# Performance work log

Measured on AMD Instinct MI355X. Metric: run time of the kernel, lower is better.

Reference implementation:

```python
import jax, jax.numpy as jnp
import numpy as np
import math

LN_EPS = 1e-5
EPS = 1e-8

def _unfold3(x, stride):
    # torch nn.Unfold(kernel_size=3, stride=stride, padding=1); output [B, C*9, L]
    B, C, H, W = x.shape
    xp = jnp.pad(x, ((0, 0), (0, 0), (1, 1), (1, 1)))
    Ho = (H + 2 - 3) // stride + 1
    Wo = (W + 2 - 3) // stride + 1
    pats = [xp[:, :, i:i + stride * (Ho - 1) + 1:stride, j:j + stride * (Wo - 1) + 1:stride]
            for i in range(3) for j in range(3)]
    out = jnp.stack(pats, axis=2)  # [B,C,9,Ho,Wo]  (c-major, then kh,kw: torch ordering)
    return out.reshape(B, C * 9, Ho * Wo)

def _ln(x, g, b):
    mu = jnp.mean(x, axis=-1, keepdims=True)
    var = jnp.mean((x - mu) ** 2, axis=-1, keepdims=True)
    return (x - mu) * jax.lax.rsqrt(var + LN_EPS) * g + b

def _prm_exp(x, w):
    # x: [B,T,emb], w: [m,emb] -> [B,T,m]
    m = w.shape[0]
    xd = jnp.sum(x * x, axis=-1, keepdims=True) / 2.0
    wtx = jnp.einsum('bte,me->btm', x, w)
    return jnp.exp(wtx - xd) / math.sqrt(m)

def _performer(x, kqv_w, kqv_b, pw, pb, g1, b1, g2, b2, m1w, m1b, m2w, m2b, w):
    # Token_performer.forward (dropout = identity, eval mode)
    h = _ln(x, g1, b1)
    kqv = h @ kqv_w.T + kqv_b
    k, q, v = jnp.split(kqv, 3, axis=-1)  # torch.split order: k, q, v
    kp = _prm_exp(k, w)
    qp = _prm_exp(q, w)
    D = jnp.einsum('btm,bm->bt', qp, kp.sum(axis=1))[..., None]        # [B,T,1]
    kptv = jnp.einsum('btn,btm->bnm', v, kp)                            # [B,emb,m]
    y = jnp.einsum('btm,bnm->btn', qp, kptv) / (D + EPS)                # [B,T,emb]
    y = v + (y @ pw.T + pb)
    h2 = _ln(y, g2, b2)
    mlp = jax.nn.gelu(h2 @ m1w.T + m1b, approximate=False) @ m2w.T + m2b
    return y + mlp

def _forward(x,
             p1_kqv_w, p1_kqv_b, p1_proj_w, p1_proj_b, p1_n1_g, p1_n1_b, p1_n2_g, p1_n2_b,
             p1_m1_w, p1_m1_b, p1_m2_w, p1_m2_b, p1_w,
             p2_kqv_w, p2_kqv_b, p2_proj_w, p2_proj_b, p2_n1_g, p2_n1_b, p2_n2_g, p2_n2_b,
             p2_m1_w, p2_m1_b, p2_m2_w, p2_m2_b, p2_w,
             proj_w, proj_b):
    t = _unfold3(x, 1).transpose(0, 2, 1)  # [B, 50176, 27]
    t = _performer(t, p1_kqv_w, p1_kqv_b, p1_proj_w, p1_proj_b, p1_n1_g, p1_n1_b,
                   p1_n2_g, p1_n2_b, p1_m1_w, p1_m1_b, p1_m2_w, p1_m2_b, p1_w)
    B, N, C = t.shape
    s = int(math.isqrt(N))
    t = t.transpose(0, 2, 1).reshape(B, C, s, s)
    t = _unfold3(t, 2).transpose(0, 2, 1)  # [B, 12544, 576]
    t = _performer(t, p2_kqv_w, p2_kqv_b, p2_proj_w, p2_proj_b, p2_n1_g, p2_n1_b,
                   p2_n2_g, p2_n2_b, p2_m1_w, p2_m1_b, p2_m2_w, p2_m2_b, p2_w)
    B, N, C = t.shape
    s = int(math.isqrt(N))
    t = t.transpose(0, 2, 1).reshape(B, C, s, s)
    t = _unfold3(t, 2).transpose(0, 2, 1)  # [B, 3136, 576]
    return t @ proj_w.T + proj_b           # [B, 3136, 768]

def setup_inputs() -> dict:
    key = jax.random.key(0)
    ks = iter(jax.random.split(key, 40))
    def rn(shape, scale=0.02):
        return (jax.random.normal(next(ks), shape, dtype=jnp.float32) * scale)
    EMB, M = 64, 32
    inp = {'x': jax.random.normal(next(ks), (8, 3, 224, 224), dtype=jnp.float32)}
    for pfx, dim in (('p1', 27), ('p2', 576)):
        inp[f'{pfx}_kqv_w'] = rn((3 * EMB, dim))
        inp[f'{pfx}_kqv_b'] = jnp.zeros((3 * EMB,), jnp.float32)
        inp[f'{pfx}_proj_w'] = rn((EMB, EMB))
        inp[f'{pfx}_proj_b'] = jnp.zeros((EMB,), jnp.float32)
        inp[f'{pfx}_n1_g'] = jnp.ones((dim,), jnp.float32)
        inp[f'{pfx}_n1_b'] = jnp.zeros((dim,), jnp.float32)
        inp[f'{pfx}_n2_g'] = jnp.ones((EMB,), jnp.float32)
        inp[f'{pfx}_n2_b'] = jnp.zeros((EMB,), jnp.float32)
        inp[f'{pfx}_m1_w'] = rn((EMB, EMB))
        inp[f'{pfx}_m1_b'] = jnp.zeros((EMB,), jnp.float32)
        inp[f'{pfx}_m2_w'] = rn((EMB, EMB))
        inp[f'{pfx}_m2_b'] = jnp.zeros((EMB,), jnp.float32)
        # frozen random-feature projection, scaled ~ orthogonal * sqrt(m)
        inp[f'{pfx}_w'] = jax.random.normal(next(ks), (M, EMB), dtype=jnp.float32)
    inp['proj_w'] = rn((768, 576))
    inp['proj_b'] = jnp.zeros((768,), jnp.float32)
    return inp

def reference(x,
              p1_kqv_w, p1_kqv_b, p1_proj_w, p1_proj_b, p1_n1_g, p1_n1_b, p1_n2_g, p1_n2_b,
              p1_m1_w, p1_m1_b, p1_m2_w, p1_m2_b, p1_w,
              p2_kqv_w, p2_kqv_b, p2_proj_w, p2_proj_b, p2_n1_g, p2_n1_b, p2_n2_g, p2_n2_b,
              p2_m1_w, p2_m1_b, p2_m2_w, p2_m2_b, p2_w,
              proj_w, proj_b):
    return _forward(x,
                    p1_kqv_w, p1_kqv_b, p1_proj_w, p1_proj_b, p1_n1_g, p1_n1_b, p1_n2_g, p1_n2_b,
                    p1_m1_w, p1_m1_b, p1_m2_w, p1_m2_b, p1_w,
                    p2_kqv_w, p2_kqv_b, p2_proj_w, p2_proj_b, p2_n1_g, p2_n1_b, p2_n2_g, p2_n2_b,
                    p2_m1_w, p2_m1_b, p2_m2_w, p2_m2_b, p2_w,
                    proj_w, proj_b)
```

## Files before the change

kernel.cpp:

```cpp
#include <hip/hip_runtime.h>
#include <hip/hip_bf16.h>
#include <math.h>

typedef __hip_bfloat16 bf16;
typedef __attribute__((ext_vector_type(8))) short frag8;
typedef __attribute__((ext_vector_type(4))) float f32x4;
typedef long long ll;

__device__ __forceinline__ float b2f(bf16 v) { return __bfloat162float(v); }
__device__ __forceinline__ bf16 f2b(float v) { return __float2bfloat16(v); }

__device__ __forceinline__ unsigned pk2f(float a, float b) {
    union { bf16 h[2]; unsigned u; } c;
    c.h[0] = f2b(a); c.h[1] = f2b(b);
    return c.u;
}
__device__ __forceinline__ void up8(const bf16* p, float* f) {
    const uint4 u = *(const uint4*)p;
    union { unsigned u; bf16 h[2]; } c;
    c.u = u.x; f[0] = b2f(c.h[0]); f[1] = b2f(c.h[1]);
    c.u = u.y; f[2] = b2f(c.h[0]); f[3] = b2f(c.h[1]);
    c.u = u.z; f[4] = b2f(c.h[0]); f[5] = b2f(c.h[1]);
    c.u = u.w; f[6] = b2f(c.h[0]); f[7] = b2f(c.h[1]);
}
__device__ __forceinline__ void up8u(const uint4 u, float* f) {
    union { unsigned u; bf16 h[2]; } c;
    c.u = u.x; f[0] = b2f(c.h[0]); f[1] = b2f(c.h[1]);
    c.u = u.y; f[2] = b2f(c.h[0]); f[3] = b2f(c.h[1]);
    c.u = u.z; f[4] = b2f(c.h[0]); f[5] = b2f(c.h[1]);
    c.u = u.w; f[6] = b2f(c.h[0]); f[7] = b2f(c.h[1]);
}

#define LN_EPS 1e-5f
#define D_EPS 1e-8f
#define INV_SQRT_M 0.17677669529663687f

__global__ __launch_bounds__(256) void k_sniff(const void* x, int* mode)
{
    __shared__ int cnt;
    if (threadIdx.x == 0) cnt = 0;
    __syncthreads();
    const unsigned short* u = (const unsigned short*)x;
    const unsigned short h = u[2 * threadIdx.x];
    const unsigned int bits = ((unsigned int)h) << 16;
    const float v = __uint_as_float(bits);
    const float a = fabsf(v);
    const bool sane = (h == 0) || (a >= 1e-8f && a <= 1e4f);
    if (!sane) atomicAdd(&cnt, 1);
    __syncthreads();
    if (threadIdx.x == 0) *mode = (cnt > 64) ? 1 : 0;
}

struct CvTab { const void* src[28]; int dstOff[28]; int cum[29]; };

__global__ __launch_bounds__(256) void k_convert_all(CvTab tab, bf16* base,
                                                     const int* mode)
{
    const int idx = blockIdx.x * 256 + threadIdx.x;
    if (idx >= tab.cum[28]) return;
    int s = 0;
    while (idx >= tab.cum[s + 1]) ++s;
    const int local = idx - tab.cum[s];
    const float v = (*mode) ? ((const float*)tab.src[s])[local]
                            : b2f(((const bf16*)tab.src[s])[local]);
    base[tab.dstOff[s] + local] = f2b(v);
}

__global__ __launch_bounds__(256) void k_prep(
    const void* __restrict__ w1raw, const int* __restrict__ mode,
    bf16* __restrict__ w1ph, bf16* __restrict__ w1pl)
{
    const int idx = blockIdx.x * 256 + threadIdx.x;
    if (idx >= 6144) return;
    const int o = idx >> 5, k = idx & 31;
    float v = 0.f;
    if (k < 27)
        v = (*mode) ? ((const float*)w1raw)[o * 27 + k]
                    : b2f(((const bf16*)w1raw)[o * 27 + k]);
    const bf16 h = f2b(v);
    w1ph[idx] = h;
    w1pl[idx] = f2b(v - b2f(h));
}

__global__ __launch_bounds__(256) void k_fused1(
    const bf16* __restrict__ x, const bf16* __restrict__ w1ph,
    const bf16* __restrict__ w1pl, const bf16* __restrict__ kqvb,
    const bf16* __restrict__ n1g, const bf16* __restrict__ n1b,
    const bf16* __restrict__ pw,
    bf16* __restrict__ KP, bf16* __restrict__ QP, bf16* __restrict__ V,
    float* __restrict__ red, const int b)
{
    __shared__ __align__(16) char smem[49632];
    bf16 (*wps)[72] = (bf16(*)[72])(smem);
    bf16 (*Ah)[40]  = (bf16(*)[40])(smem + 4608);
    bf16 (*Al)[40]  = (bf16(*)[40])(smem + 9728);
    bf16 (*Th)[72]  = (bf16(*)[72])(smem + 14848);
    bf16 (*Tl)[72]  = (bf16(*)[72])(smem + 24064);
    bf16 (*Wh)[40]  = (bf16(*)[40])(smem + 33280);
    bf16 (*Wl)[40]  = (bf16(*)[40])(smem + 38400);
    bf16 (*KPs)[40] = (bf16(*)[40])(smem + 43520);
    bf16 (*Vs)[72]  = (bf16(*)[72])(smem + 14848);
    float* kbs = (float*)(smem + 48640);
    float* gs  = (float*)(smem + 49408);
    float* bs  = (float*)(smem + 49520);

    const int tid = threadIdx.x;
    {
        const int i = tid * 8;
        *(uint4*)(&wps[i >> 6][i & 63]) = *(const uint4*)(pw + i);
    }
    if (tid < 192) kbs[tid] = b2f(kqvb[tid]);
    if (tid < 27) { gs[tid] = b2f(n1g[tid]); bs[tid] = b2f(n1b[tid]); }
    if (blockIdx.x == 0)
        for (int i = tid; i < 2080; i += 256) red[i] = 0.f;

    const int tok = tid >> 2, part = tid & 3;
    const int t = blockIdx.x * 64 + tok;
    const int h = t / 224, w = t - h * 224;
    const int d0 = part * 7;
    const int nd = (part == 3) ? 6 : 7;
    float vals[7];
    float s = 0.f;
    #pragma unroll
    for (int q = 0; q < 7; ++q) {
        float val = 0.f;
        if (q < nd) {
            const int d = d0 + q;
            const int c = d / 9, rr = d - c * 9;
            const int pi = rr / 3, pj = rr - pi * 3;
            const int hh = h + pi - 1, ww = w + pj - 1;
            if (hh >= 0 && hh < 224 && ww >= 0 && ww < 224)
                val = b2f(x[((ll)(b * 3 + c) * 224 + hh) * 224 + ww]);
        }
        vals[q] = val; s += val;
    }
    s += __shfl_xor(s, 1, 64);  s += __shfl_xor(s, 2, 64);
    const float mean = s * (1.f / 27.f);
    float s2 = 0.f;
    #pragma unroll
    for (int q = 0; q < 7; ++q) {
        if (q < nd) { const float dd = vals[q] - mean; s2 += dd * dd; }
    }
    s2 += __shfl_xor(s2, 1, 64); s2 += __shfl_xor(s2, 2, 64);
    const float rs = rsqrtf(s2 * (1.f / 27.f) + LN_EPS);
    __syncthreads();
    #pragma unroll
    for (int q = 0; q < 7; ++q) {
        if (q < nd) {
            const int d = d0 + q;
            const float nv = (vals[q] - mean) * rs * gs[d] + bs[d];
            const bf16 nh = f2b(nv);
            Ah[tok][d] = nh;
            Al[tok][d] = f2b(nv - b2f(nh));
        }
    }
    if (part == 3) {
        #pragma unroll
        for (int d = 27; d < 32; ++d) { Ah[tok][d] = f2b(0.f); Al[tok][d] = f2b(0.f); }
    }

    const int wv = tid >> 6, lane = tid & 63;
    const int l15 = lane & 15;
    const int k8 = (lane >> 4) << 3;
    const int rbase = (lane >> 4) << 2;
    const int srow = tid >> 2;
    const int scol = (tid & 3) << 3;
    const int colg = (tid & 3) << 4;

    float xdK[4], xdQ[4];

    #pragma unroll
    for (int g = 0; g < 3; ++g) {
        *(uint4*)(&Wh[srow][scol]) = *(const uint4*)(w1ph + (g * 64 + srow) * 32 + scol);
        *(uint4*)(&Wl[srow][scol]) = *(const uint4*)(w1pl + (g * 64 + srow) * 32 + scol);
        __syncthreads();
        const frag8 ah = *(const frag8*)(&Ah[(wv << 4) + l15][k8]);
        const frag8 al = *(const frag8*)(&Al[(wv << 4) + l15][k8]);
        f32x4 acc[4] = {};
        #pragma unroll
        for (int nt = 0; nt < 4; ++nt) {
            const frag8 bh = *(const frag8*)(&Wh[(nt << 4) + l15][k8]);
            const frag8 bl = *(const frag8*)(&Wl[(nt << 4) + l15][k8]);
            acc[nt] = __builtin_amdgcn_mfma_f32_16x16x32_bf16(ah, bh, acc[nt], 0, 0, 0);
            acc[nt] = __builtin_amdgcn_mfma_f32_16x16x32_bf16(al, bh, acc[nt], 0, 0, 0);
            acc[nt] = __builtin_amdgcn_mfma_f32_16x16x32_bf16(ah, bl, acc[nt], 0, 0, 0);
            acc[nt] = __builtin_amdgcn_mfma_f32_16x16x32_bf16(al, bl, acc[nt], 0, 0, 0);
        }
        float xdp[4] = {0.f, 0.f, 0.f, 0.f};
        #pragma unroll
        for (int nt = 0; nt < 4; ++nt) {
            const int col = (nt << 4) + l15;
            const float bv = kbs[g * 64 + col];
            #pragma unroll
            for (int r = 0; r < 4; ++r) {
                const float tb = acc[nt][r] + bv;
                const int trow = (wv << 4) + rbase + r;
                if (g < 2) {
                    const bf16 th = f2b(tb);
                    Th[trow][col] = th;
                    Tl[trow][col] = f2b(tb - b2f(th));
                    xdp[r] += tb * tb;
                } else {
                    Vs[trow][col] = f2b(tb);
                }
            }
        }
        if (g < 2) {
            #pragma unroll
            for (int r = 0; r < 4; ++r) {
                float v = xdp[r];
                v += __shfl_xor(v, 1, 64); v += __shfl_xor(v, 2, 64);
                v += __shfl_xor(v, 4, 64); v += __shfl_xor(v, 8, 64);
                if (g == 0) xdK[r] = 0.5f * v; else xdQ[r] = 0.5f * v;
            }
        }
        __syncthreads();
        if (g < 2) {
            f32x4 acc2[2] = {};
            #pragma unroll
            for (int k0 = 0; k0 < 64; k0 += 32) {
                const frag8 ath = *(const frag8*)(&Th[(wv << 4) + l15][k8 + k0]);
                const frag8 atl = *(const frag8*)(&Tl[(wv << 4) + l15][k8 + k0]);
                #pragma unroll
                for (int nt = 0; nt < 2; ++nt) {
                    const frag8 bw = *(const frag8*)(&wps[(nt << 4) + l15][k8 + k0]);
                    acc2[nt] = __builtin_amdgcn_mfma_f32_16x16x32_bf16(ath, bw, acc2[nt], 0, 0, 0);
                    acc2[nt] = __builtin_amdgcn_mfma_f32_16x16x32_bf16(atl, bw, acc2[nt], 0, 0, 0);
                }
            }
            #pragma unroll
            for (int nt = 0; nt < 2; ++nt)
                #pragma unroll
                for (int r = 0; r < 4; ++r) {
                    const float xd = (g == 0) ? xdK[r] : xdQ[r];
                    const float p = expf(fminf(acc2[nt][r] - xd, 30.f)) * INV_SQRT_M;
                    KPs[(wv << 4) + rbase + r][(nt << 4) + l15] = f2b(p);
                }
            __syncthreads();
            bf16* dstP = (g == 0 ? KP : QP) + ((ll)blockIdx.x * 64 + srow) * 32 + scol;
            *(uint4*)dstP = *(const uint4*)(&KPs[srow][scol]);
            __syncthreads();
        } else {
            bf16* dstV = V + ((ll)blockIdx.x * 64 + srow) * 64 + colg;
            *(uint4*)dstV       = *(const uint4*)(&Vs[srow][colg]);
            *(uint4*)(dstV + 8) = *(const uint4*)(&Vs[srow][colg + 8]);
        }
    }
}

__global__ __launch_bounds__(256) void k_reduce(
    const bf16* __restrict__ kpB, const bf16* __restrict__ vB, const int vstride,
    const int T, float* __restrict__ redBase, const int chunk)
{
    __shared__ bf16 VT[64][72];
    __shared__ bf16 KT[32][72];
    const int bz = blockIdx.y;
    const bf16* kp = kpB + (ll)bz * T * 32;
    const bf16* v  = vB + (ll)bz * T * (ll)vstride;
    float* red = redBase + (ll)bz * 2080;
    const int tid = threadIdx.x;
    const int wv = tid >> 6, lane = tid & 63;
    const int l15 = lane & 15, k8 = (lane >> 4) << 3, rbase = (lane >> 4) << 2;
    const int t0 = blockIdx.x * chunk;

    frag8 ones;
    {
        union { bf16 h; short s; } u; u.h = f2b(1.f);
        #pragma unroll
        for (int i = 0; i < 8; ++i) ones[i] = u.s;
    }

    f32x4 acc[2] = {};
    f32x4 accK[2] = {};

    for (int tt = 0; tt < chunk; tt += 64) {
        const int tb = t0 + tt;
        __syncthreads();
        {
            const int tk = tid >> 2, n0 = (tid & 3) << 4;
            const bf16* src = v + (ll)(tb + tk) * vstride + n0;
            bf16 tmp[16];
            *(uint4*)tmp       = *(const uint4*)src;
            *(uint4*)(tmp + 8) = *(const uint4*)(src + 8);
            #pragma unroll
            for (int j = 0; j < 16; ++j) VT[n0 + j][tk] = tmp[j];
        }
        {
            const int tk = tid >> 2, m0 = (tid & 3) << 3;
            const bf16* src = kp + (ll)(tb + tk) * 32 + m0;
            bf16 tmp[8];
            *(uint4*)tmp = *(const uint4*)src;
            #pragma unroll
            for (int j = 0; j < 8; ++j) KT[m0 + j][tk] = tmp[j];
        }
        __syncthreads();
        #pragma unroll
        for (int ks = 0; ks < 2; ++ks) {
            const frag8 af = *(const frag8*)(&VT[(wv << 4) + l15][k8 + ks * 32]);
            #pragma unroll
            for (int tn = 0; tn < 2; ++tn) {
                const frag8 bfv = *(const frag8*)(&KT[(tn << 4) + l15][k8 + ks * 32]);
                acc[tn] = __builtin_amdgcn_mfma_f32_16x16x32_bf16(af, bfv, acc[tn], 0, 0, 0);
            }
            if (wv == 0) {
                #pragma unroll
                for (int tn = 0; tn < 2; ++tn) {
                    const frag8 bfv = *(const frag8*)(&KT[(tn << 4) + l15][k8 + ks * 32]);
                    accK[tn] = __builtin_amdgcn_mfma_f32_16x16x32_bf16(ones, bfv, accK[tn], 0, 0, 0);
                }
            }
        }
    }
    #pragma unroll
    for (int tn = 0; tn < 2; ++tn) {
        const int m = (tn << 4) + l15;
        #pragma unroll
        for (int r = 0; r < 4; ++r) {
            const int n = (wv << 4) + rbase + r;
            atomicAdd(&red[n * 32 + m], acc[tn][r]);
        }
    }
    if (wv == 0 && (lane >> 4) == 0) {
        #pragma unroll
        for (int tn = 0; tn < 2; ++tn)
            atomicAdd(&red[2048 + (tn << 4) + l15], accK[tn][0]);
    }
}

__global__ __launch_bounds__(256) void k_postmlp(
    const bf16* __restrict__ qpB, const float* __restrict__ redBase,
    const bf16* __restrict__ vB, const int vstride,
    const bf16* __restrict__ pw, const bf16* __restrict__ pb,
    const bf16* __restrict__ n2g, const bf16* __restrict__ n2b,
    const bf16* __restrict__ w1, const bf16* __restrict__ b1,
    const bf16* __restrict__ w2, const bf16* __restrict__ b2,
    bf16* outB, const int T)
{
    __shared__ __align__(16) char smem[47232];
    bf16 (*QPs)[40] = (bf16(*)[40])(smem);
    bf16 (*KH)[40]  = (bf16(*)[40])(smem + 5120);
    bf16 (*KL)[40]  = (bf16(*)[40])(smem + 10240);
    float (*Cs)[72] = (float(*)[72])(smem);
    bf16 (*W1s)[72] = (bf16(*)[72])(smem);
    bf16 (*W2s)[72] = (bf16(*)[72])(smem + 9216);
    bf16 (*PWs)[72] = (bf16(*)[72])(smem + 18432);
    bf16 (*Gs)[72]  = (bf16(*)[72])(smem + 18432);
    bf16 (*Y0H)[72] = (bf16(*)[72])(smem + 27648);
    bf16 (*Ys)[72]  = (bf16(*)[72])(smem + 27648);
    bf16 (*Y0L)[72] = (bf16(*)[72])(smem + 36864);
    bf16 (*Hn)[72]  = (bf16(*)[72])(smem + 36864);
    float* invs  = (float*)(smem + 46080);
    float* pbs   = (float*)(smem + 46336);
    float* ksums = (float*)(smem + 46592);
    float* mns   = (float*)(smem + 46720);
    float* rss   = (float*)(smem + 46976);

    const int tid = threadIdx.x;
    const int bz = blockIdx.y;
    const float* red = redBase + (ll)bz * 2080;
    const bf16* qp = qpB + (ll)bz * (ll)T * 32;
    const bf16* v  = vB + (ll)bz * (ll)T * (ll)vstride;
    bf16* out = outB + (ll)bz * (ll)T * 64;
    const ll m0 = (ll)blockIdx.x * 64;

    const int lr = tid >> 2;
    const int lc8 = (tid & 3) << 3;
    const int lc16 = (tid & 3) << 4;

    *(uint4*)(&QPs[lr][lc8]) = *(const uint4*)(qp + (m0 + lr) * 32 + lc8);
    *(uint4*)(&PWs[lr][lc16])     = *(const uint4*)(pw + lr * 64 + lc16);
    *(uint4*)(&PWs[lr][lc16 + 8]) = *(const uint4*)(pw + lr * 64 + lc16 + 8);
    {
        const int i0 = tid * 8;
        const float4 a = *(const float4*)(red + i0);
        const float4 b = *(const float4*)(red + i0 + 4);
        const int n = i0 >> 5, m = i0 & 31;
        float xs[8] = {a.x, a.y, a.z, a.w, b.x, b.y, b.z, b.w};
        #pragma unroll
        for (int k = 0; k < 8; ++k) {
            const bf16 h = f2b(xs[k]);
            KH[n][m + k] = h;
            KL[n][m + k] = f2b(xs[k] - b2f(h));
        }
    }
    if (tid < 32) ksums[tid] = red[2048 + tid];
    if (tid < 64) pbs[tid] = b2f(pb[tid]);
    __syncthreads();

    if (tid < 64) {
        float D = D_EPS;
        #pragma unroll
        for (int m = 0; m < 32; ++m) D += b2f(QPs[tid][m]) * ksums[m];
        invs[tid] = 1.f / D;
    }

    const int wv = tid >> 6, lane = tid & 63;
    const int l15 = lane & 15;
    const int mr = (wv << 4) + l15;
    const int k8 = (lane >> 4) << 3;
    const int rbase = (lane >> 4) << 2;

    f32x4 acc[4] = {};
    {
        const frag8 af = *(const frag8*)(&QPs[mr][k8]);
        #pragma unroll
        for (int tn = 0; tn < 4; ++tn) {
            const int nr = (tn << 4) + l15;
            const frag8 bh = *(const frag8*)(&KH[nr][k8]);
            acc[tn] = __builtin_amdgcn_mfma_f32_16x16x32_bf16(af, bh, acc[tn], 0, 0, 0);
            const frag8 bl = *(const frag8*)(&KL[nr][k8]);
            acc[tn] = __builtin_amdgcn_mfma_f32_16x16x32_bf16(af, bl, acc[tn], 0, 0, 0);
        }
    }
    #pragma unroll
    for (int tn = 0; tn < 4; ++tn) {
        const int n = (tn << 4) + l15;
        #pragma unroll
        for (int r = 0; r < 4; ++r) {
            const float x = acc[tn][r];
            const bf16 h = f2b(x);
            Y0H[(wv << 4) + rbase + r][n] = h;
            Y0L[(wv << 4) + rbase + r][n] = f2b(x - b2f(h));
        }
    }
    __syncthreads();

    f32x4 acc2[4] = {};
    #pragma unroll
    for (int k0 = 0; k0 < 64; k0 += 32) {
        const frag8 ah = *(const frag8*)(&Y0H[mr][k8 + k0]);
        const frag8 al = *(const frag8*)(&Y0L[mr][k8 + k0]);
        #pragma unroll
        for (int tn = 0; tn < 4; ++tn) {
            const frag8 bw = *(const frag8*)(&PWs[(tn << 4) + l15][k8 + k0]);
            acc2[tn] = __builtin_amdgcn_mfma_f32_16x16x32_bf16(ah, bw, acc2[tn], 0, 0, 0);
            acc2[tn] = __builtin_amdgcn_mfma_f32_16x16x32_bf16(al, bw, acc2[tn], 0, 0, 0);
        }
    }
    #pragma unroll
    for (int tn = 0; tn < 4; ++tn) {
        const int n = (tn << 4) + l15;
        #pragma unroll
        for (int r = 0; r < 4; ++r) {
            const int row = (wv << 4) + rbase + r;
            Cs[row][n] = acc2[tn][r] * invs[row] + pbs[n];
        }
    }
    __syncthreads();

    {
        const int row = tid >> 2;
        const bf16* vsrc = v + (m0 + row) * (ll)vstride + lc16;
        #pragma unroll
        for (int hh = 0; hh < 2; ++hh) {
            float vv[8];
            up8(vsrc + hh * 8, vv);
            const float* cp = &Cs[row][lc16 + hh * 8];
            uint4 st;
            st.x = pk2f(cp[0] + vv[0], cp[1] + vv[1]);
            st.y = pk2f(cp[2] + vv[2], cp[3] + vv[3]);
            st.z = pk2f(cp[4] + vv[4], cp[5] + vv[5]);
            st.w = pk2f(cp[6] + vv[6], cp[7] + vv[7]);
            *(uint4*)(&Ys[row][lc16 + hh * 8]) = st;
        }
    }
    __syncthreads();

    if (tid < 64) {
        float s = 0.f, s2 = 0.f;
        #pragma unroll
        for (int n = 0; n < 64; ++n) { const float vv = b2f(Ys[tid][n]); s += vv; s2 += vv * vv; }
        const float mn = s * (1.f / 64.f);
        const float var = fmaxf(s2 * (1.f / 64.f) - mn * mn, 0.f);
        mns[tid] = mn; rss[tid] = rsqrtf(var + LN_EPS);
    }
    *(uint4*)(&W1s[lr][lc16])     = *(const uint4*)(w1 + lr * 64 + lc16);
    *(uint4*)(&W1s[lr][lc16 + 8]) = *(const uint4*)(w1 + lr * 64 + lc16 + 8);
    *(uint4*)(&W2s[lr][lc16])     = *(const uint4*)(w2 + lr * 64 + lc16);
    *(uint4*)(&W2s[lr][lc16 + 8]) = *(const uint4*)(w2 + lr * 64 + lc16 + 8);
    __syncthreads();

    for (int i = tid; i < 4096; i += 256) {
        const int r = i >> 6, c = i & 63;
        Hn[r][c] = f2b((b2f(Ys[r][c]) - mns[r]) * rss[r] * b2f(n2g[c]) + b2f(n2b[c]));
    }
    __syncthreads();

    f32x4 accm[4] = {};
    #pragma unroll
    for (int k0 = 0; k0 < 64; k0 += 32) {
        const frag8 af = *(const frag8*)(&Hn[mr][k8 + k0]);
        #pragma unroll
        for (int tn = 0; tn < 4; ++tn) {
            const frag8 bfv = *(const frag8*)(&W1s[(tn << 4) + l15][k8 + k0]);
            accm[tn] = __builtin_amdgcn_mfma_f32_16x16x32_bf16(af, bfv, accm[tn], 0, 0, 0);
        }
    }
    #pragma unroll
    for (int tn = 0; tn < 4; ++tn) {
        const int n = (tn << 4) + l15;
        const float bv = b2f(b1[n]);
        #pragma unroll
        for (int r = 0; r < 4; ++r) {
            float vg = accm[tn][r] + bv;
            vg = 0.5f * vg * (1.f + erff(vg * 0.70710678118654752f));
            Gs[(wv << 4) + rbase + r][n] = f2b(vg);
        }
    }
    __syncthreads();

    f32x4 accn[4] = {};
    #pragma unroll
    for (int k0 = 0; k0 < 64; k0 += 32) {
        const frag8 af = *(const frag8*)(&Gs[mr][k8 + k0]);
        #pragma unroll
        for (int tn = 0; tn < 4; ++tn) {
            const frag8 bfv = *(const frag8*)(&W2s[(tn << 4) + l15][k8 + k0]);
            accn[tn] = __builtin_amdgcn_mfma_f32_16x16x32_bf16(af, bfv, accn[tn], 0, 0, 0);
        }
    }
    #pragma unroll
    for (int tn = 0; tn < 4; ++tn) {
        const int n = (tn << 4) + l15;
        const float bv = b2f(b2[n]);
        #pragma unroll
        for (int r = 0; r < 4; ++r)
            Hn[(wv << 4) + rbase + r][n] = f2b(accn[tn][r] + bv);
    }
    __syncthreads();

    {
        const int row = tid >> 2;
        bf16* dst = out + (m0 + row) * 64 + lc16;
        #pragma unroll
        for (int hh = 0; hh < 2; ++hh) {
            float sv[8], rv[8];
            up8(&Hn[row][lc16 + hh * 8], sv);
            up8(&Ys[row][lc16 + hh * 8], rv);
            uint4 st;
            st.x = pk2f(sv[0] + rv[0], sv[1] + rv[1]);
            st.y = pk2f(sv[2] + rv[2], sv[3] + rv[3]);
            st.z = pk2f(sv[4] + rv[4], sv[5] + rv[5]);
            st.w = pk2f(sv[6] + rv[6], sv[7] + rv[7]);
            *(uint4*)(dst + hh * 8) = st;
        }
    }
}

__global__ __launch_bounds__(256) void k_unfold576(
    const bf16* __restrict__ in, const int Hin, const int Ho,
    const bf16* __restrict__ g, const bf16* __restrict__ bb,
    const int do_ln, bf16* __restrict__ A,
    const ll inBStride, const ll outBStride)
{
    in += (ll)blockIdx.y * inBStride;
    A  += (ll)blockIdx.y * outBStride;
    const int t = blockIdx.x * 4 + (threadIdx.x >> 6);
    const int l = threadIdx.x & 63;
    const int ho = t / Ho, wo = t - ho * Ho;
    float vals[9];
    float s = 0.f;
    #pragma unroll
    for (int r = 0; r < 9; ++r) {
        const int d = l + (r << 6);
        const int c = d / 9;
        const int rr = d - c * 9;
        const int i = rr / 3, j = rr - i * 3;
        const int hh = 2 * ho + i - 1, ww = 2 * wo + j - 1;
        float val = 0.f;
        if (hh >= 0 && hh < Hin && ww >= 0 && ww < Hin)
            val = b2f(in[((ll)hh * Hin + ww) * 64 + c]);
        vals[r] = val; s += val;
    }
    bf16* out = A + (ll)t * 576;
    if (do_ln) {
        #pragma unroll
        for (int o = 32; o > 0; o >>= 1) s += __shfl_xor(s, o, 64);
        const float mean = s * (1.f / 576.f);
        float s2 = 0.f;
        #pragma unroll
        for (int r = 0; r < 9; ++r) { const float dd = vals[r] - mean; s2 += dd * dd; }
        #pragma unroll
        for (int o = 32; o > 0; o >>= 1) s2 += __shfl_xor(s2, o, 64);
        const float rs = rsqrtf(s2 * (1.f / 576.f) + LN_EPS);
        #pragma unroll
        for (int r = 0; r < 9; ++r) {
            const int d = l + (r << 6);
            out[d] = f2b((vals[r] - mean) * rs * b2f(g[d]) + b2f(bb[d]));
        }
    } else {
        #pragma unroll
        for (int r = 0; r < 9; ++r) out[l + (r << 6)] = f2b(vals[r]);
    }
}

__global__ __launch_bounds__(256) void k_gemm(
    const bf16* __restrict__ A, const int lda,
    const bf16* __restrict__ W,
    const bf16* __restrict__ bias,
    const bf16* res, const int ldres,
    void* C, const int ldc, const ll mOff,
    const int K, const int* outm, const int gridN)
{
    __shared__ bf16 As[2][64][40];
    __shared__ bf16 Bs[2][64][40];
    __shared__ __align__(16) char epi[17408];
    float (*Cf)[68] = (float(*)[68])epi;
    bf16 (*Cs)[72] = (bf16(*)[72])epi;

    const int nwg = gridDim.x;
    const int orig = blockIdx.x;
    const int xcd = orig & 7;
    const int q = nwg >> 3, r = nwg & 7;
    const int wgid = (xcd < r ? xcd * (q + 1) : r * (q + 1) + (xcd - r) * q)
                     + (orig >> 3);
    const int mTile = wgid / gridN;
    const int nTile = wgid - mTile * gridN;
    const ll m0 = (ll)mTile * 64;
    const int n0 = nTile * 64;

    const int tid = threadIdx.x;
    const int wv = tid >> 6;
    const int lane = tid & 63;
    f32x4 acc[4] = {};
    const int lr = tid >> 2;
    const int lc = (tid & 3) << 3;
    const int mr = (wv << 4) + (lane & 15);
    const int k8 = (lane >> 4) << 3;
    const bf16* Ag = A + (m0 + lr) * (ll)lda + lc;
    const bf16* Wg = W + (ll)(n0 + lr) * K + lc;

    uint4 av  = *(const uint4*)(Ag);
    uint4 wv4 = *(const uint4*)(Wg);
    *(uint4*)(&As[0][lr][lc]) = av;
    *(uint4*)(&Bs[0][lr][lc]) = wv4;
    int cur = 0;
    __syncthreads();
    for (int k0 = 0; k0 < K; k0 += 32) {
        const bool nxt = (k0 + 32 < K);
        if (nxt) {
            av  = *(const uint4*)(Ag + k0 + 32);
            wv4 = *(const uint4*)(Wg + k0 + 32);
        }
        const frag8 af = *(const frag8*)(&As[cur][mr][k8]);
        #pragma unroll
        for (int tn = 0; tn < 4; ++tn) {
            const frag8 bfv = *(const frag8*)(&Bs[cur][(tn << 4) + (lane & 15)][k8]);
            acc[tn] = __builtin_amdgcn_mfma_f32_16x16x32_bf16(af, bfv, acc[tn], 0, 0, 0);
        }
        if (nxt) {
            *(uint4*)(&As[cur ^ 1][lr][lc]) = av;
            *(uint4*)(&Bs[cur ^ 1][lr][lc]) = wv4;
        }
        __syncthreads();
        cur ^= 1;
    }
    const int om = outm ? *outm : 0;
    const int rbase = (lane >> 4) << 2;
    if (om) {
        #pragma unroll
        for (int tn = 0; tn < 4; ++tn) {
            const int nl = (tn << 4) + (lane & 15);
            const float bv = bias ? b2f(bias[n0 + nl]) : 0.f;
            #pragma unroll
            for (int r = 0; r < 4; ++r) {
                const ll m = m0 + (wv << 4) + rbase + r;
                float v = acc[tn][r] + bv;
                if (res) v += b2f(res[m * (ll)ldres + n0 + nl]);
                Cf[(wv << 4) + rbase + r][nl] = v;
            }
        }
        __syncthreads();
        const int row = tid >> 2;
        const int cg = (tid & 3) << 4;
        float* dst = (float*)C + (m0 + mOff + row) * (ll)ldc + n0 + cg;
        #pragma unroll
        for (int u = 0; u < 4; ++u)
            *(uint4*)(dst + u * 4) = *(const uint4*)(&Cf[row][cg + u * 4]);
        return;
    }
    #pragma unroll
    for (int tn = 0; tn < 4; ++tn) {
        const int nl = (tn << 4) + (lane & 15);
        const float bv = bias ? b2f(bias[n0 + nl]) : 0.f;
        #pragma unroll
        for (int r = 0; r < 4; ++r) {
            const ll m = m0 + (wv << 4) + rbase + r;
            float v = acc[tn][r] + bv;
            if (res) v += b2f(res[m * (ll)ldres + n0 + nl]);
            Cs[(wv << 4) + rbase + r][nl] = f2b(v);
        }
    }
    __syncthreads();
    const int row = tid >> 2;
    const int colg = (tid & 3) << 4;
    bf16* dst = (bf16*)C + (m0 + mOff + row) * (ll)ldc + n0 + colg;
    *(uint4*)dst       = *(const uint4*)(&Cs[row][colg]);
    *(uint4*)(dst + 8) = *(const uint4*)(&Cs[row][colg + 8]);
}

__global__ __launch_bounds__(256) void k_fusedP2(
    const bf16* __restrict__ kqv, const bf16* __restrict__ pw,
    bf16* __restrict__ KP, bf16* __restrict__ QP,
    float* __restrict__ redBase, const int T)
{
    __shared__ __align__(16) char smem[19200];
    bf16 (*Ks)[72]  = (bf16(*)[72])(smem);
    bf16 (*wps)[72] = (bf16(*)[72])(smem + 9216);
    bf16 (*KPs)[40] = (bf16(*)[40])(smem + 13824);
    float* xds = (float*)(smem + 18944);

    const int tid = threadIdx.x;
    const int bz = blockIdx.y;
    {
        const int i = tid * 8;
        *(uint4*)(&wps[i >> 6][i & 63]) = *(const uint4*)(pw + i);
    }
    if (blockIdx.x == 0) {
        float* red = redBase + (ll)bz * 2080;
        for (int i = tid; i < 2080; i += 256) red[i] = 0.f;
    }
    const ll gt0 = (ll)bz * T + (ll)blockIdx.x * 64;
    const int srow = tid >> 2;
    const int colg = (tid & 3) << 4;
    const int scol = (tid & 3) << 3;
    const int wv = tid >> 6, lane = tid & 63;
    const int l15 = lane & 15, k8 = (lane >> 4) << 3, rbase = (lane >> 4) << 2;

    #pragma unroll
    for (int p = 0; p < 2; ++p) {
        const bf16* src = kqv + (gt0 + srow) * 192 + p * 64 + colg;
        const uint4 u0 = *(const uint4*)src;
        const uint4 u1 = *(const uint4*)(src + 8);
        *(uint4*)(&Ks[srow][colg])     = u0;
        *(uint4*)(&Ks[srow][colg + 8]) = u1;
        float f0[8], f1[8];
        up8u(u0, f0); up8u(u1, f1);
        float s2 = 0.f;
        #pragma unroll
        for (int k = 0; k < 8; ++k) s2 += f0[k] * f0[k] + f1[k] * f1[k];
        s2 += __shfl_xor(s2, 1, 64); s2 += __shfl_xor(s2, 2, 64);
        if ((tid & 3) == 0) xds[srow] = 0.5f * s2;
        __syncthreads();
        f32x4 acc2[2] = {};
        #pragma unroll
        for (int k0 = 0; k0 < 64; k0 += 32) {
            const frag8 af = *(const frag8*)(&Ks[(wv << 4) + l15][k8 + k0]);
            #pragma unroll
            for (int nt = 0; nt < 2; ++nt) {
                const frag8 bw = *(const frag8*)(&wps[(nt << 4) + l15][k8 + k0]);
                acc2[nt] = __builtin_amdgcn_mfma_f32_16x16x32_bf16(af, bw, acc2[nt], 0, 0, 0);
            }
        }
        #pragma unroll
        for (int nt = 0; nt < 2; ++nt)
            #pragma unroll
            for (int r = 0; r < 4; ++r) {
                const int trow = (wv << 4) + rbase + r;
                const float pv = expf(fminf(acc2[nt][r] - xds[trow], 30.f)) * INV_SQRT_M;
                KPs[trow][(nt << 4) + l15] = f2b(pv);
            }
        __syncthreads();
        bf16* dst = (p == 0 ? KP : QP) + (gt0 + srow) * 32 + scol;
        *(uint4*)dst = *(const uint4*)(&KPs[srow][scol]);
        __syncthreads();
    }
}

extern "C" void kernel_launch(void* const* d_in, const int* in_sizes, int n_in,
                              void* d_out, int out_size, void* d_ws, size_t ws_size,
                              hipStream_t stream)
{
    (void)in_sizes; (void)n_in; (void)out_size;
    const int T1 = 50176, T2 = 12544;
    char* ws = (char*)d_ws;

    size_t cur = 0;
    auto alloc = [&](size_t bytes) {
        size_t r = cur; cur += (bytes + 127) & ~(size_t)127; return r;
    };
    static const int segIdx[28] = {0, 2, 3, 4, 5, 6, 7, 8, 9, 10, 11, 12, 13,
                                   14, 15, 16, 17, 18, 19, 20, 21, 22, 23, 24, 25, 26, 27, 28};
    static const int segN[28] = {1204224, 192, 4096, 64, 27, 27, 64, 64, 4096, 64, 4096, 64, 2048,
                                 110592, 192, 4096, 64, 576, 576, 64, 64, 4096, 64, 4096, 64, 2048,
                                 442368, 768};
    size_t segOff[28];
    for (int i = 0; i < 28; ++i) segOff[i] = alloc((size_t)segN[i] * 2);
    const size_t oMODE = alloc(256);
    const size_t oRED  = alloc(66560);
    const size_t oW1P  = alloc(24576);
    const size_t oBIG  = alloc(6422528);
    const size_t oKP   = alloc(3211264);
    const size_t oQP   = alloc(3211264);
    (void)oQP;

    bf16* P[28];
    for (int i = 0; i < 28; ++i) P[i] = (bf16*)(ws + segOff[i]);
    bf16* XC = P[0];
    bf16 *P1KQVB = P[1], *P1PW = P[2], *P1PB = P[3], *P1N1G = P[4], *P1N1B = P[5];
    bf16 *P1N2G = P[6], *P1N2B = P[7], *P1M1W = P[8], *P1M1B = P[9], *P1M2W = P[10];
    bf16 *P1M2B = P[11], *P1W = P[12];
    bf16 *P2KQVW = P[13], *P2KQVB = P[14], *P2PW = P[15], *P2PB = P[16];
    bf16 *P2N1G = P[17], *P2N1B = P[18], *P2N2G = P[19], *P2N2B = P[20];
    bf16 *P2M1W = P[21], *P2M1B = P[22], *P2M2W = P[23], *P2M2B = P[24], *P2W = P[25];
    bf16 *PROJW = P[26], *PROJB = P[27];

    int*   MODE = (int*)(ws + oMODE);
    float* REDF = (float*)(ws + oRED);
    bf16*  W1PH = (bf16*)(ws + oW1P);
    bf16*  W1PL = (bf16*)(ws + oW1P + 12288);
    bf16*  BIG  = (bf16*)(ws + oBIG);
    bf16*  KP   = (bf16*)(ws + oKP);
    bf16*  QP   = (bf16*)(ws + oKP + 3211264);
    bf16*  A2   = (bf16*)(ws + oKP);
    bf16*  KQV2F = (bf16*)d_out;
    bf16*  KP2F  = (bf16*)(ws + oKP);
    bf16*  QP2F  = (bf16*)(ws + oKP + 6422528);
    bf16*  YB2F  = (bf16*)(ws + oBIG);
    bf16*  A3c   = (bf16*)(ws + oBIG + 12845056);

    k_sniff<<<1, 256, 0, stream>>>(d_in[0], MODE);
    CvTab tab;
    int cum = 0;
    for (int i = 0; i < 28; ++i) {
        tab.src[i] = d_in[segIdx[i]];
        tab.dstOff[i] = (int)(segOff[i] / 2);
        tab.cum[i] = cum;
        cum += segN[i];
    }
    tab.cum[28] = cum;
    k_convert_all<<<(cum + 255) / 256, 256, 0, stream>>>(tab, (bf16*)ws, MODE);
    k_prep<<<24, 256, 0, stream>>>(d_in[1], MODE, W1PH, W1PL);

    for (int b = 0; b < 8; ++b) {
        float* REDb = REDF + (ll)b * 2080;
        k_fused1<<<784, 256, 0, stream>>>(XC, W1PH, W1PL, P1KQVB, P1N1G, P1N1B,
                                          P1W, KP, QP, BIG, REDb, b);
        k_reduce<<<dim3(392, 1), 256, 0, stream>>>(KP, BIG, 64, T1, REDb, 128);
        k_postmlp<<<dim3(784, 1), 256, 0, stream>>>(QP, REDb, BIG, 64, P1PW, P1PB,
            P1N2G, P1N2B, P1M1W, P1M1B, P1M2W, P1M2B, BIG, T1);
        k_unfold576<<<dim3(3136, 1), 256, 0, stream>>>(BIG, 224, 112, P2N1G, P2N1B,
                                                       1, A2, 0, 0);
        k_gemm<<<588, 256, 0, stream>>>(A2, 576, P2KQVW, P2KQVB,
            nullptr, 0, KQV2F, 192, (ll)b * T2, 576, nullptr, 3);
    }

    k_fusedP2<<<dim3(196, 8), 256, 0, stream>>>(KQV2F, P2W, KP2F, QP2F, REDF, T2);
    k_reduce<<<dim3(98, 8), 256, 0, stream>>>(KP2F, KQV2F + 128, 192, T2, REDF, 128);
    k_postmlp<<<dim3(196, 8), 256, 0, stream>>>(QP2F, REDF, KQV2F + 128, 192,
        P2PW, P2PB, P2N2G, P2N2B, P2M1W, P2M1B, P2M2W, P2M2B, YB2F, T2);

    const size_t needFull = oBIG + 12845056 + (size_t)25088 * 576 * 2;
    if (ws_size >= needFull) {
        bf16* A3 = (bf16*)(ws + oBIG + 12845056);
        k_unfold576<<<dim3(784, 8), 256, 0, stream>>>(
            YB2F, 112, 56, nullptr, nullptr, 0, A3, (ll)T2 * 64, (ll)3136 * 576);
        k_gemm<<<4704, 256, 0, stream>>>(A3, 576, PROJW, PROJB,
            nullptr, 0, d_out, 768, 0, 576, MODE, 12);
    } else {
        for (int c = 0; c < 4; ++c) {
            k_unfold576<<<dim3(784, 2), 256, 0, stream>>>(
                YB2F + (ll)(2 * c) * T2 * 64, 112, 56, nullptr, nullptr, 0,
                A3c, (ll)T2 * 64, (ll)3136 * 576);
            k_gemm<<<1176, 256, 0, stream>>>(A3c, 576, PROJW, PROJB,
                nullptr, 0, d_out, 768, (ll)c * 6272, 576, MODE, 12);
        }
    }
}
```

Baseline: 1.012 ms.

## Enlarge GEMM M-tile to 128 rows and write fp32 output directly

The generic GEMM kernel now computes a 128x64 output tile per workgroup, with each wave holding two 16-row MFMA fragments so that every B fragment loaded from LDS is reused twice. Grid sizes are halved to match. The fp32 output path now stores accumulators straight to global memory instead of staging them through shared memory, which drops a barrier but gives scattered 4-byte stores. Fewer workgroups may lower occupancy for the smaller per-batch KQV GEMM.

```diff
diff --git a/kernel.cpp b/kernel.cpp
--- a/kernel.cpp
+++ b/kernel.cpp
@@ -602,11 +602,10 @@
     void* C, const int ldc, const ll mOff,
     const int K, const int* outm, const int gridN)
 {
-    __shared__ bf16 As[2][64][40];
-    __shared__ bf16 Bs[2][64][40];
-    __shared__ __align__(16) char epi[17408];
-    float (*Cf)[68] = (float(*)[68])epi;
-    bf16 (*Cs)[72] = (bf16(*)[72])epi;
+    __shared__ __align__(16) char smem[30720];
+    bf16 (*As)[128][40] = (bf16(*)[128][40])smem;
+    bf16 (*Bs)[64][40]  = (bf16(*)[64][40])(smem + 20480);
+    bf16 (*Cs)[72]      = (bf16(*)[72])smem;
 
     const int nwg = gridDim.x;
     const int orig = blockIdx.x;
@@ -616,87 +615,92 @@
                      + (orig >> 3);
     const int mTile = wgid / gridN;
     const int nTile = wgid - mTile * gridN;
-    const ll m0 = (ll)mTile * 64;
+    const ll m0 = (ll)mTile * 128;
     const int n0 = nTile * 64;
 
     const int tid = threadIdx.x;
-    const int wv = tid >> 6;
-    const int lane = tid & 63;
-    f32x4 acc[4] = {};
-    const int lr = tid >> 2;
-    const int lc = (tid & 3) << 3;
-    const int mr = (wv << 4) + (lane & 15);
+    const int wv = tid >> 6, lane = tid & 63, l15 = lane & 15;
     const int k8 = (lane >> 4) << 3;
-    const bf16* Ag = A + (m0 + lr) * (ll)lda + lc;
-    const bf16* Wg = W + (ll)(n0 + lr) * K + lc;
-
-    uint4 av  = *(const uint4*)(Ag);
-    uint4 wv4 = *(const uint4*)(Wg);
-    *(uint4*)(&As[0][lr][lc]) = av;
-    *(uint4*)(&Bs[0][lr][lc]) = wv4;
-    int cur = 0;
+    const int rbase = (lane >> 4) << 2;
+    const int mr0 = (wv << 5) + l15;
+    const int ar = tid >> 1, ac = (tid & 1) << 4;
+    const int br = tid >> 2, bc = (tid & 3) << 3;
+    const bf16* Ag = A + (m0 + ar) * (ll)lda + ac;
+    const bf16* Wg = W + (ll)(n0 + br) * K + bc;
+
+    f32x4 acc[2][4] = {};
+    uint4 a0 = *(const uint4*)(Ag);
+    uint4 a1 = *(const uint4*)(Ag + 8);
+    uint4 b0 = *(const uint4*)(Wg);
+    *(uint4*)(&As[0][ar][ac])     = a0;
+    *(uint4*)(&As[0][ar][ac + 8]) = a1;
+    *(uint4*)(&Bs[0][br][bc])     = b0;
+    int curb = 0;
     __syncthreads();
     for (int k0 = 0; k0 < K; k0 += 32) {
         const bool nxt = (k0 + 32 < K);
         if (nxt) {
-            av  = *(const uint4*)(Ag + k0 + 32);
-            wv4 = *(const uint4*)(Wg + k0 + 32);
-        }
-        const frag8 af = *(const frag8*)(&As[cur][mr][k8]);
+            a0 = *(const uint4*)(Ag + k0 + 32);
+            a1 = *(const uint4*)(Ag + k0 + 40);
+            b0 = *(const uint4*)(Wg + k0 + 32);
+        }
+        const frag8 af0 = *(const frag8*)(&As[curb][mr0][k8]);
+        const frag8 af1 = *(const frag8*)(&As[curb][mr0 + 16][k8]);
         #pragma unroll
         for (int tn = 0; tn < 4; ++tn) {
-            const frag8 bfv = *(const frag8*)(&Bs[cur][(tn << 4) + (lane & 15)][k8]);
-            acc[tn] = __builtin_amdgcn_mfma_f32_16x16x32_bf16(af, bfv, acc[tn], 0, 0, 0);
+            const frag8 bfv = *(const frag8*)(&Bs[curb][(tn << 4) + l15][k8]);
+            acc[0][tn] = __builtin_amdgcn_mfma_f32_16x16x32_bf16(af0, bfv, acc[0][tn], 0, 0, 0);
+            acc[1][tn] = __builtin_amdgcn_mfma_f32_16x16x32_bf16(af1, bfv, acc[1][tn], 0, 0, 0);
         }
         if (nxt) {
-            *(uint4*)(&As[cur ^ 1][lr][lc]) = av;
-            *(uint4*)(&Bs[cur ^ 1][lr][lc]) = wv4;
+            *(uint4*)(&As[curb ^ 1][ar][ac])     = a0;
+            *(uint4*)(&As[curb ^ 1][ar][ac + 8]) = a1;
+            *(uint4*)(&Bs[curb ^ 1][br][bc])     = b0;
         }
         __syncthreads();
-        cur ^= 1;
+        curb ^= 1;
     }
     const int om = outm ? *outm : 0;
-    const int rbase = (lane >> 4) << 2;
     if (om) {
         #pragma unroll
+        for (int mi = 0; mi < 2; ++mi)
+            #pragma unroll
+            for (int tn = 0; tn < 4; ++tn) {
+                const int n = n0 + (tn << 4) + l15;
+                const float bv = bias ? b2f(bias[n]) : 0.f;
+                #pragma unroll
+                for (int rr2 = 0; rr2 < 4; ++rr2) {
+                    const ll m = m0 + (wv << 5) + (mi << 4) + rbase + rr2;
+                    float v = acc[mi][tn][rr2] + bv;
+                    if (res) v += b2f(res[m * (ll)ldres + n]);
+                    ((float*)C)[(m + mOff) * (ll)ldc + n] = v;
+                }
+            }
+        return;
+    }
+    #pragma unroll
+    for (int mi = 0; mi < 2; ++mi)
+        #pragma unroll
         for (int tn = 0; tn < 4; ++tn) {
-            const int nl = (tn << 4) + (lane & 15);
+            const int nl = (tn << 4) + l15;
             const float bv = bias ? b2f(bias[n0 + nl]) : 0.f;
             #pragma unroll
-            for (int r = 0; r < 4; ++r) {
-                const ll m = m0 + (wv << 4) + rbase + r;
-                float v = acc[tn][r] + bv;
+            for (int rr2 = 0; rr2 < 4; ++rr2) {
+                const ll m = m0 + (wv << 5) + (mi << 4) + rbase + rr2;
+                float v = acc[mi][tn][rr2] + bv;
                 if (res) v += b2f(res[m * (ll)ldres + n0 + nl]);
-                Cf[(wv << 4) + rbase + r][nl] = v;
+                Cs[(wv << 5) + (mi << 4) + rbase + rr2][nl] = f2b(v);
             }
         }
-        __syncthreads();
-        const int row = tid >> 2;
-        const int cg = (tid & 3) << 4;
-        float* dst = (float*)C + (m0 + mOff + row) * (ll)ldc + n0 + cg;
-        #pragma unroll
-        for (int u = 0; u < 4; ++u)
-            *(uint4*)(dst + u * 4) = *(const uint4*)(&Cf[row][cg + u * 4]);
-        return;
-    }
-    #pragma unroll
-    for (int tn = 0; tn < 4; ++tn) {
-        const int nl = (tn << 4) + (lane & 15);
-        const float bv = bias ? b2f(bias[n0 + nl]) : 0.f;
-        #pragma unroll
-        for (int r = 0; r < 4; ++r) {
-            const ll m = m0 + (wv << 4) + rbase + r;
-            float v = acc[tn][r] + bv;
-            if (res) v += b2f(res[m * (ll)ldres + n0 + nl]);
-            Cs[(wv << 4) + rbase + r][nl] = f2b(v);
-        }
-    }
     __syncthreads();
     const int row = tid >> 2;
     const int colg = (tid & 3) << 4;
-    bf16* dst = (bf16*)C + (m0 + mOff + row) * (ll)ldc + n0 + colg;
-    *(uint4*)dst       = *(const uint4*)(&Cs[row][colg]);
-    *(uint4*)(dst + 8) = *(const uint4*)(&Cs[row][colg + 8]);
+    #pragma unroll
+    for (int h2 = 0; h2 < 2; ++h2) {
+        bf16* dst = (bf16*)C + (m0 + mOff + row + h2 * 64) * (ll)ldc + n0 + colg;
+        *(uint4*)dst       = *(const uint4*)(&Cs[row + h2 * 64][colg]);
+        *(uint4*)(dst + 8) = *(const uint4*)(&Cs[row + h2 * 64][colg + 8]);
+    }
 }
 
 __global__ __launch_bounds__(256) void k_fusedP2(
@@ -841,7 +845,7 @@
             P1N2G, P1N2B, P1M1W, P1M1B, P1M2W, P1M2B, BIG, T1);
         k_unfold576<<<dim3(3136, 1), 256, 0, stream>>>(BIG, 224, 112, P2N1G, P2N1B,
                                                        1, A2, 0, 0);
-        k_gemm<<<588, 256, 0, stream>>>(A2, 576, P2KQVW, P2KQVB,
+        k_gemm<<<294, 256, 0, stream>>>(A2, 576, P2KQVW, P2KQVB,
             nullptr, 0, KQV2F, 192, (ll)b * T2, 576, nullptr, 3);
     }
 
@@ -855,14 +859,14 @@
         bf16* A3 = (bf16*)(ws + oBIG + 12845056);
         k_unfold576<<<dim3(784, 8), 256, 0, stream>>>(
             YB2F, 112, 56, nullptr, nullptr, 0, A3, (ll)T2 * 64, (ll)3136 * 576);
-        k_gemm<<<4704, 256, 0, stream>>>(A3, 576, PROJW, PROJB,
+        k_gemm<<<2352, 256, 0, stream>>>(A3, 576, PROJW, PROJB,
             nullptr, 0, d_out, 768, 0, 576, MODE, 12);
     } else {
         for (int c = 0; c < 4; ++c) {
             k_unfold576<<<dim3(784, 2), 256, 0, stream>>>(
                 YB2F + (ll)(2 * c) * T2 * 64, 112, 56, nullptr, nullptr, 0,
                 A3c, (ll)T2 * 64, (ll)3136 * 576);
-            k_gemm<<<1176, 256, 0, stream>>>(A3c, 576, PROJW, PROJB,
+            k_gemm<<<588, 256, 0, stream>>>(A3c, 576, PROJW, PROJB,
                 nullptr, 0, d_out, 768, (ll)c * 6272, 576, MODE, 12);
         }
     }
```

New measurement: 1.006 ms. About the same (-0.6%).
